# Kernel optimization log

Hardware: AMD Instinct MI355X
Metric: run time of the kernel (lower is better)

The kernel has to match this reference:

```python
import jax, jax.numpy as jnp
import numpy as np

SHIFT = 1  # torch module picks shift_direction in {-1,+1} randomly; fixed to +1 for determinism
K = 9      # unfold kernel height
PAD = 4    # unfold padding along H


def setup_inputs() -> dict:
    key = jax.random.key(0)
    k1, k2, k3 = jax.random.split(key, 3)
    x = jax.random.normal(k1, (1, 24, 56, 56), dtype=jnp.float32)
    w0 = jax.random.normal(k2, (96, 9, 14), dtype=jnp.float32)   # weights[0]
    w1 = jax.random.normal(k3, (24, 2, 14), dtype=jnp.float32)   # weights[1]
    return {"x": x, "w0": w0, "w1": w1}


def reference(x, w0, w1):
    # einsum 'limn, ikj -> lmnkj': (1,24,56,56) x (24,2,14) -> (1,56,56,2,14)
    t = jnp.einsum('limn,ikj->lmnkj', x, w1)
    # view as NCHW with C=56, H=56, W=28 for unfold(kernel=(9,1), padding=(4,0))
    t = t.reshape(1, 56, 56, 28)
    tp = jnp.pad(t, ((0, 0), (0, 0), (PAD, PAD), (0, 0)))
    # unfold along H: windows[:, c, kh, h, w] = padded[:, c, h + kh, w]
    win = jnp.stack([tp[:, :, i:i + 56, :] for i in range(K)], axis=2)  # (1,56,9,56,28)
    # merge (56,2) -> 112 (last 28 = 2*14), roll along that merged axis, split back, sum over the 2-axis
    t = win.reshape(1, 56, K, 112, 14)
    t = jnp.roll(t, SHIFT, axis=3)
    t = t.reshape(1, 56, K, 56, 2, 14).sum(axis=4)  # (1,56,9,56,14)
    # einsum 'lmjnk, ijk -> limn': (1,56,9,56,14) x (96,9,14) -> (1,96,56,56)
    return jnp.einsum('lmjnk,ijk->limn', t, w0)
```

## Files before the change

kernel.cpp:

```cpp
#include <hip/hip_runtime.h>


#define MDIM 56
#define NDIM 56
#define CIN  24
#define JD   14
#define KHD  9
#define IOUT 96
#define ITILE 24
#define BP   15

__global__ __launch_bounds__(256) void fused_shift_conv(
    const float* __restrict__ x,
    const float* __restrict__ w0,
    const float* __restrict__ w1,
    float* __restrict__ out)
{
    const int m     = blockIdx.x;
    const int itile = blockIdx.y;
    const int tid   = threadIdx.x;

    __shared__ float sx[CIN * MDIM];
    __shared__ float sw1[CIN * 2 * JD];
    __shared__ float sw0[ITILE * KHD * JD];
    __shared__ float sB[2 * 64 * BP];

    for (int e = tid; e < CIN * MDIM; e += 256) {
        int c = e / MDIM, h = e % MDIM;
        sx[e] = x[(c * MDIM + m) * NDIM + h];
    }
    for (int e = tid; e < CIN * 2 * JD; e += 256)
        sw1[e] = w1[e];
    for (int e = tid; e < ITILE * KHD * JD; e += 256)
        sw0[e] = w0[itile * ITILE * KHD * JD + e];
    for (int e = tid; e < 2 * 64 * BP; e += 256)
        sB[e] = 0.0f;
    __syncthreads();

    for (int e = tid; e < 2 * MDIM * JD; e += 256) {
        int k = e / (MDIM * JD);
        int r = e % (MDIM * JD);
        int h = r / JD;
        int j = r % JD;
        float acc = 0.0f;
        #pragma unroll
        for (int c = 0; c < CIN; ++c)
            acc += sx[c * MDIM + h] * sw1[(c * 2 + k) * JD + j];
        sB[(k * 64 + (h + 4)) * BP + j] = acc;
    }
    __syncthreads();

    for (int e = tid; e < ITILE * NDIM; e += 256) {
        int il = e / NDIM;
        int n  = e % NDIM;
        int h1 = (n + 55) % 56;
        const float* b0  = &sB[(0 * 64 + n ) * BP];
        const float* b1  = &sB[(1 * 64 + h1) * BP];
        const float* w0r = &sw0[il * KHD * JD];
        float acc = 0.0f;
        #pragma unroll
        for (int kh = 0; kh < KHD; ++kh) {
            #pragma unroll
            for (int j = 0; j < JD; ++j) {
                acc += w0r[kh * JD + j] * (b1[kh * BP + j] + b0[kh * BP + j]);
            }
        }
        int i = itile * ITILE + il;
        out[(i * MDIM + m) * NDIM + n] = acc;
    }
}

extern "C" void kernel_launch(void* const* d_in, const int* in_sizes, int n_in,
                              void* d_out, int out_size, void* d_ws, size_t ws_size,
                              hipStream_t stream) {
    const float* x  = (const float*)d_in[0];
    const float* w0 = (const float*)d_in[1];
    const float* w1 = (const float*)d_in[2];
    float* out = (float*)d_out;

    dim3 grid(MDIM, IOUT / ITILE);
    dim3 block(256);
    fused_shift_conv<<<grid, block, 0, stream>>>(x, w0, w1, out);
}
```

Before: 78.48 us.

## Precompute shifted window sums and register-tile output over channels and columns

Adds a shared-memory stage that sums the two shifted unfold rows once per (kh,n,j), so the main contraction no longer repeats that add for every output channel. The final contraction is then register-tiled: each thread computes a 3-channel by 2-column block, reusing each loaded window value and weight several times to cut shared-memory loads per FMA. Only 224 of 256 threads take part in the final stage, and the extra sS buffer raises shared-memory use per block and adds a barrier.

```diff
diff --git a/kernel.cpp b/kernel.cpp
--- a/kernel.cpp
+++ b/kernel.cpp
@@ -9,6 +9,11 @@
 #define IOUT 96
 #define ITILE 24
 #define BP   15
+
+#define TIL 3
+#define TNN 2
+#define NGRP (ITILE / TIL)
+#define NBLK (NDIM / TNN)
 
 __global__ __launch_bounds__(256) void fused_shift_conv(
     const float* __restrict__ x,
@@ -24,6 +29,7 @@
     __shared__ float sw1[CIN * 2 * JD];
     __shared__ float sw0[ITILE * KHD * JD];
     __shared__ float sB[2 * 64 * BP];
+    __shared__ float sS[KHD * NDIM * BP];
 
     for (int e = tid; e < CIN * MDIM; e += 256) {
         int c = e / MDIM, h = e % MDIM;
@@ -50,23 +56,57 @@
     }
     __syncthreads();
 
-    for (int e = tid; e < ITILE * NDIM; e += 256) {
-        int il = e / NDIM;
-        int n  = e % NDIM;
+    for (int e = tid; e < KHD * NDIM * JD; e += 256) {
+        int kh = e / (NDIM * JD);
+        int r  = e % (NDIM * JD);
+        int n  = r / JD;
+        int j  = r % JD;
         int h1 = (n + 55) % 56;
-        const float* b0  = &sB[(0 * 64 + n ) * BP];
-        const float* b1  = &sB[(1 * 64 + h1) * BP];
-        const float* w0r = &sw0[il * KHD * JD];
-        float acc = 0.0f;
+        sS[(kh * NDIM + n) * BP + j] =
+            sB[(0 * 64 + (n  + kh)) * BP + j] +
+            sB[(1 * 64 + (h1 + kh)) * BP + j];
+    }
+    __syncthreads();
+
+    if (tid < NGRP * NBLK) {
+        const int il0 = TIL * (tid % NGRP);
+        const int n0  = TNN * (tid / NGRP);
+
+        float acc[TIL][TNN];
+        #pragma unroll
+        for (int a = 0; a < TIL; ++a)
+            #pragma unroll
+            for (int b = 0; b < TNN; ++b)
+                acc[a][b] = 0.0f;
+
+        const float* w0a = &sw0[(il0 + 0) * KHD * JD];
+        const float* w0b = &sw0[(il0 + 1) * KHD * JD];
+        const float* w0c = &sw0[(il0 + 2) * KHD * JD];
+
         #pragma unroll
         for (int kh = 0; kh < KHD; ++kh) {
+            const float* s0 = &sS[(kh * NDIM + n0) * BP];
+            const float* s1 = s0 + BP;
+            const float* wa = w0a + kh * JD;
+            const float* wb = w0b + kh * JD;
+            const float* wc = w0c + kh * JD;
             #pragma unroll
             for (int j = 0; j < JD; ++j) {
-                acc += w0r[kh * JD + j] * (b1[kh * BP + j] + b0[kh * BP + j]);
+                float v0 = s0[j], v1 = s1[j];
+                float a0 = wa[j], a1 = wb[j], a2 = wc[j];
+                acc[0][0] += a0 * v0;  acc[0][1] += a0 * v1;
+                acc[1][0] += a1 * v0;  acc[1][1] += a1 * v1;
+                acc[2][0] += a2 * v0;  acc[2][1] += a2 * v1;
             }
         }
-        int i = itile * ITILE + il;
-        out[(i * MDIM + m) * NDIM + n] = acc;
+
+        #pragma unroll
+        for (int a = 0; a < TIL; ++a) {
+            int i = itile * ITILE + il0 + a;
+            float* o = &out[(i * MDIM + m) * NDIM + n0];
+            o[0] = acc[a][0];
+            o[1] = acc[a][1];
+        }
     }
 }
 
```

Result: faster. 72.13 us (-8.1%).

## Register-tile both contraction stages and precompute shifted window sums in shared memory

Applied to the files above, without the earlier changes.

Global loads become float4 vectorised, and the first einsum is register-tiled so each thread computes 2 rows by 4 columns of the intermediate. A new stage precomputes the summed, shifted windows (b0+b1) into a shared buffer, so the final contraction no longer redoes that add for every output channel. The final stage register-tiles 3 output channels by 2 columns per thread and writes float2 stores. This cuts shared-memory traffic and redundant adds, at the cost of more shared memory, one extra barrier, and fewer active threads in the last stage (224 of 256).

```diff
diff --git a/kernel.cpp b/kernel.cpp
--- a/kernel.cpp
+++ b/kernel.cpp
@@ -5,10 +5,12 @@
 #define NDIM 56
 #define CIN  24
 #define JD   14
+#define KJD  28
 #define KHD  9
 #define IOUT 96
 #define ITILE 24
-#define BP   15
+#define TIL 3
+#define TNN 2
 
 __global__ __launch_bounds__(256) void fused_shift_conv(
     const float* __restrict__ x,
@@ -20,53 +22,103 @@
     const int itile = blockIdx.y;
     const int tid   = threadIdx.x;
 
-    __shared__ float sx[CIN * MDIM];
-    __shared__ float sw1[CIN * 2 * JD];
-    __shared__ float sw0[ITILE * KHD * JD];
-    __shared__ float sB[2 * 64 * BP];
+    __shared__ __align__(16) float sx [CIN * MDIM];
+    __shared__ __align__(16) float sw1[CIN * KJD];
+    __shared__ __align__(16) float sw0[ITILE * KHD * JD];
+    __shared__ __align__(16) float sB [64 * KJD];
+    __shared__ __align__(16) float sS [KHD * NDIM * JD];
 
-    for (int e = tid; e < CIN * MDIM; e += 256) {
-        int c = e / MDIM, h = e % MDIM;
-        sx[e] = x[(c * MDIM + m) * NDIM + h];
-    }
-    for (int e = tid; e < CIN * 2 * JD; e += 256)
-        sw1[e] = w1[e];
-    for (int e = tid; e < ITILE * KHD * JD; e += 256)
-        sw0[e] = w0[itile * ITILE * KHD * JD + e];
-    for (int e = tid; e < 2 * 64 * BP; e += 256)
-        sB[e] = 0.0f;
-    __syncthreads();
+    {
+        float4*       sx4  = (float4*)sx;
+        float4*       sw14 = (float4*)sw1;
+        float4*       sw04 = (float4*)sw0;
+        float4*       sB4  = (float4*)sB;
+        const float4* x4   = (const float4*)x;
+        const float4* w14  = (const float4*)w1;
+        const float4* w04  = (const float4*)w0;
 
-    for (int e = tid; e < 2 * MDIM * JD; e += 256) {
-        int k = e / (MDIM * JD);
-        int r = e % (MDIM * JD);
-        int h = r / JD;
-        int j = r % JD;
-        float acc = 0.0f;
-        #pragma unroll
-        for (int c = 0; c < CIN; ++c)
-            acc += sx[c * MDIM + h] * sw1[(c * 2 + k) * JD + j];
-        sB[(k * 64 + (h + 4)) * BP + j] = acc;
+        for (int e = tid; e < CIN * JD; e += 256) {
+            int c = e / JD, t = e % JD;
+            sx4[e] = x4[c * 784 + m * JD + t];
+        }
+        for (int e = tid; e < (CIN * KJD) / 4; e += 256)
+            sw14[e] = w14[e];
+        for (int e = tid; e < (ITILE * KHD * JD) / 4; e += 256)
+            sw04[e] = w04[itile * (ITILE * KHD * JD / 4) + e];
+        for (int e = tid; e < 56; e += 256) {
+            int r = e / 7;
+            int hp = r + (r >= 4 ? 56 : 0);
+            sB4[hp * 7 + (e % 7)] = make_float4(0.f, 0.f, 0.f, 0.f);
+        }
     }
     __syncthreads();
 
-    for (int e = tid; e < ITILE * NDIM; e += 256) {
-        int il = e / NDIM;
-        int n  = e % NDIM;
+    if (tid < 196) {
+        const int g   = tid / 7;
+        const int q   = tid % 7;
+        const int h0  = 2 * g;
+        const int kj0 = 4 * q;
+
+        float4 acc0 = make_float4(0.f, 0.f, 0.f, 0.f);
+        float4 acc1 = make_float4(0.f, 0.f, 0.f, 0.f);
+        #pragma unroll
+        for (int c = 0; c < CIN; ++c) {
+            float2 xv = *(const float2*)&sx[c * MDIM + h0];
+            float4 wv = *(const float4*)&sw1[c * KJD + kj0];
+            acc0.x += xv.x * wv.x;  acc0.y += xv.x * wv.y;
+            acc0.z += xv.x * wv.z;  acc0.w += xv.x * wv.w;
+            acc1.x += xv.y * wv.x;  acc1.y += xv.y * wv.y;
+            acc1.z += xv.y * wv.z;  acc1.w += xv.y * wv.w;
+        }
+        *(float4*)&sB[(h0 + 4) * KJD + kj0] = acc0;
+        *(float4*)&sB[(h0 + 5) * KJD + kj0] = acc1;
+    }
+    __syncthreads();
+
+    for (int e = tid; e < KHD * NDIM * 7; e += 256) {
+        int kh = e / (NDIM * 7);
+        int r  = e % (NDIM * 7);
+        int n  = r / 7;
+        int j2 = 2 * (r % 7);
         int h1 = (n + 55) % 56;
-        const float* b0  = &sB[(0 * 64 + n ) * BP];
-        const float* b1  = &sB[(1 * 64 + h1) * BP];
-        const float* w0r = &sw0[il * KHD * JD];
-        float acc = 0.0f;
+        float2 a = *(const float2*)&sB[(n  + kh) * KJD + j2];
+        float2 b = *(const float2*)&sB[(h1 + kh) * KJD + JD + j2];
+        *(float2*)&sS[(kh * NDIM + n) * JD + j2] = make_float2(a.x + b.x, a.y + b.y);
+    }
+    __syncthreads();
+
+    if (tid < (ITILE / TIL) * (NDIM / TNN)) {
+        const int il0 = TIL * (tid % (ITILE / TIL));
+        const int n0  = TNN * (tid / (ITILE / TIL));
+
+        float acc[TIL][TNN] = {};
+
         #pragma unroll
         for (int kh = 0; kh < KHD; ++kh) {
+            const float2* s0 = (const float2*)&sS[(kh * NDIM + n0    ) * JD];
+            const float2* s1 = (const float2*)&sS[(kh * NDIM + n0 + 1) * JD];
+            const float2* wa = (const float2*)&sw0[((il0 + 0) * KHD + kh) * JD];
+            const float2* wb = (const float2*)&sw0[((il0 + 1) * KHD + kh) * JD];
+            const float2* wc = (const float2*)&sw0[((il0 + 2) * KHD + kh) * JD];
             #pragma unroll
-            for (int j = 0; j < JD; ++j) {
-                acc += w0r[kh * JD + j] * (b1[kh * BP + j] + b0[kh * BP + j]);
+            for (int j2 = 0; j2 < 7; ++j2) {
+                float2 v0 = s0[j2], v1 = s1[j2];
+                float2 A = wa[j2], B = wb[j2], C = wc[j2];
+                acc[0][0] += A.x * v0.x + A.y * v0.y;
+                acc[0][1] += A.x * v1.x + A.y * v1.y;
+                acc[1][0] += B.x * v0.x + B.y * v0.y;
+                acc[1][1] += B.x * v1.x + B.y * v1.y;
+                acc[2][0] += C.x * v0.x + C.y * v0.y;
+                acc[2][1] += C.x * v1.x + C.y * v1.y;
             }
         }
-        int i = itile * ITILE + il;
-        out[(i * MDIM + m) * NDIM + n] = acc;
+
+        #pragma unroll
+        for (int a = 0; a < TIL; ++a) {
+            int i = itile * ITILE + il0 + a;
+            *(float2*)&out[(i * MDIM + m) * NDIM + n0] =
+                make_float2(acc[a][0], acc[a][1]);
+        }
     }
 }
 
```

Measured after the change: 65.46 us. -16.6%, faster.
